# Kernel tuning notes

Hardware: AMD Instinct MI355X
Metric: run time of the kernel (lower is better)

The kernel has to match this reference:

```python
import jax, jax.numpy as jnp
import numpy as np
from string import ascii_letters as ABC

N = 12
DIM = 2 ** N
_s = 1.0 / np.sqrt(2.0)
# measurement-basis rotations for X, Y, Z
U_BASIS = jnp.asarray(np.stack([
    np.array([[1, 1], [1, -1]]) * _s,
    np.array([[1, -1j], [1, 1j]]) * _s,
    np.eye(2),
]), dtype=jnp.complex64)


def build_H(params_x, params_zz):
    """Dense transverse-field Ising Hamiltonian: sum_i x_i X_i + sum_i zz_i Z_i Z_{i+1}."""
    basis = jnp.arange(DIM)
    bits = (basis[:, None] >> jnp.arange(N)[None, :]) & 1          # (DIM, N)
    signs = (1 - 2 * bits).astype(jnp.float32)                      # Z eigenvalues
    zz_diag = (signs[:, :-1] * signs[:, 1:]) @ params_zz            # (DIM,)
    flips = basis[:, None] ^ (1 << jnp.arange(N))[None, :]          # (DIM, N)
    rows = jnp.repeat(basis, N)
    cols = flips.reshape(-1)
    vals = jnp.tile(params_x, DIM).astype(jnp.complex64)
    H = jnp.zeros((DIM, DIM), jnp.complex64).at[rows, cols].add(vals)
    return H + jnp.diag(zz_diag.astype(jnp.complex64))


def setup_inputs() -> dict:
    key = jax.random.key(0)
    k1, k2, k3, k4, k5 = jax.random.split(key, 5)
    return {
        "initial_state": 0,
        "ts": jax.random.uniform(k1, (8,), dtype=jnp.float32),
        "pauli_obs": jax.random.randint(k2, (32, N), 0, 3),
        "indices": jax.random.randint(k3, (8, 32, 256), 0, DIM),
        "params_x": jax.random.normal(k4, (N,), dtype=jnp.float32),
        "params_zz": jax.random.normal(k5, (N - 1,), dtype=jnp.float32),
    }


def reference(initial_state, ts, pauli_obs, indices, params_x, params_zz):
    H = build_H(params_x, params_zz)
    rots = U_BASIS[pauli_obs]                    # (B, N, 2, 2)
    ops = [rots[:, i] for i in range(N)]
    subs = ','.join([ABC[1:1 + N]] + [f'a{ABC[1 + N + i]}{ABC[1 + i]}' for i in range(N)]) \
        + '->a' + ABC[1 + N:1 + 2 * N]
    B = pauli_obs.shape[0]

    def one_t(args):
        t, idx = args
        U = jax.scipy.linalg.expm((-1j) * t.astype(jnp.complex64) * H)
        fs = U[:, initial_state].reshape([2] * N)          # state tensor
        rot_state = jnp.einsum(subs, fs, *ops)             # (B, 2, ..., 2)
        probs = jnp.abs(rot_state.reshape(B, DIM)) ** 2    # (B, DIM)
        return jnp.take_along_axis(probs, idx, axis=1)     # (B, shots)

    return jax.lax.map(one_t, (ts, indices))               # (T, B, shots)
```

## Files before the change

### kernel.cpp

```cpp
#include <hip/hip_runtime.h>
#include <math.h>

#define QN 12
#define QDIM 4096
#define CHEB_TOL 2e-3f
#define LSZ (QDIM + 2 * (QDIM / 16))

template <int CTRL>
__device__ __forceinline__ float dppf(float x) {
    int v = __builtin_amdgcn_update_dpp(0, __float_as_int(x), CTRL, 0xF, 0xF, false);
    return __int_as_float(v);
}
#define DPP_QX1 0xB1
#define DPP_QX2 0x4E
#define DPP_QX3 0x1B
#define DPP_HM  0x141
#define DPP_R8  0x128
__device__ __forceinline__ float dpp_x1(float x) { return dppf<DPP_QX1>(x); }
__device__ __forceinline__ float dpp_x2(float x) { return dppf<DPP_QX2>(x); }
__device__ __forceinline__ float dpp_x4(float x) { return dppf<DPP_HM>(dppf<DPP_QX3>(x)); }
__device__ __forceinline__ float dpp_x8(float x) { return dppf<DPP_R8>(x); }

#define CHEB_STEP(T1, T2, CURB, NXTB, KVAL, FVAL, ODD, WRITEB)                \
    {                                                                          \
        const int   k_ = (KVAL);                                               \
        const float f_ = (FVAL);                                               \
        float4 nbv[6][2];                                                      \
        _Pragma("unroll")                                                      \
        for (int j = 6; j < QN; ++j) {                                         \
            const int gx = g0 ^ (1 << j);                                      \
            const int hx = h0 ^ (1 << (j - 4));                                \
            const float4* q4 = (const float4*)((CURB) + gx + 2 * hx);          \
            nbv[j - 6][0] = q4[0];                                             \
            nbv[j - 6][1] = q4[1];                                             \
        }                                                                      \
        float hr[4], hi[4];                                                    \
        _Pragma("unroll")                                                      \
        for (int e = 0; e < 4; ++e) {                                          \
            hr[e] = dg[e] * T1[e].x + xj[0] * T1[e ^ 1].x                      \
                  + xj[1] * T1[e ^ 2].x;                                       \
            hi[e] = dg[e] * T1[e].y + xj[0] * T1[e ^ 1].y                      \
                  + xj[1] * T1[e ^ 2].y;                                       \
            hr[e] += xj[2] * dpp_x1(T1[e].x);  hi[e] += xj[2] * dpp_x1(T1[e].y); \
            hr[e] += xj[3] * dpp_x2(T1[e].x);  hi[e] += xj[3] * dpp_x2(T1[e].y); \
            hr[e] += xj[4] * dpp_x4(T1[e].x);  hi[e] += xj[4] * dpp_x4(T1[e].y); \
            hr[e] += xj[5] * dpp_x8(T1[e].x);  hi[e] += xj[5] * dpp_x8(T1[e].y); \
        }                                                                      \
        _Pragma("unroll")                                                      \
        for (int j = 6; j < QN; ++j) {                                         \
            _Pragma("unroll")                                                  \
            for (int m = 0; m < 2; ++m) {                                      \
                hr[2 * m]     += xj[j] * nbv[j - 6][m].x;                      \
                hi[2 * m]     += xj[j] * nbv[j - 6][m].y;                      \
                hr[2 * m + 1] += xj[j] * nbv[j - 6][m].z;                      \
                hi[2 * m + 1] += xj[j] * nbv[j - 6][m].w;                      \
            }                                                                  \
        }                                                                      \
        const float Jk2 = 2.0f * Jc[k_];                                       \
        const float c_  = (k_ & 2) ? Jk2 : -Jk2;                               \
        _Pragma("unroll")                                                      \
        for (int e = 0; e < 4; ++e) {                                          \
            const float tnx = f_ * hr[e] - T2[e].x;                            \
            const float tny = f_ * hi[e] - T2[e].y;                            \
            T2[e].x = tnx; T2[e].y = tny;                                      \
            if (ODD) {                                                         \
                acc[e].x = fmaf(-c_, tny, acc[e].x);                           \
                acc[e].y = fmaf( c_, tnx, acc[e].y);                           \
            } else {                                                           \
                acc[e].x = fmaf(-c_, tnx, acc[e].x);                           \
                acc[e].y = fmaf(-c_, tny, acc[e].y);                           \
            }                                                                  \
        }                                                                      \
        if (WRITEB) {                                                          \
            float4* w_ = (float4*)((NXTB) + l0);                               \
            w_[0] = make_float4(T2[0].x, T2[0].y, T2[1].x, T2[1].y);           \
            w_[1] = make_float4(T2[2].x, T2[2].y, T2[3].x, T2[3].y);           \
            __syncthreads();                                                   \
        }                                                                      \
    }

__global__ __launch_bounds__(1024) void evolve_kernel(
    const int* __restrict__ init_state,
    const float* __restrict__ ts,
    const float* __restrict__ params_x,
    const float* __restrict__ params_zz,
    float2* __restrict__ psi_out)
{
    __shared__ __align__(16) float2 bufA[LSZ];
    __shared__ __align__(16) float2 bufB[LSZ];
    __shared__ float  Jc[128];
    __shared__ float  suLDS[160];
    __shared__ int    dsh;

    const int tid = threadIdx.x;
    const int tI  = blockIdx.x;
    const float t = ts[tI];
    const int g0 = tid * 4;
    const int h0 = g0 >> 4;
    const int l0 = g0 + 2 * h0;

    if (tid < 160) suLDS[tid] = 0.f;

    float xj[QN];
    float bound = 0.f;
#pragma unroll
    for (int j = 0; j < QN; ++j) { xj[j] = params_x[j]; bound += fabsf(xj[j]); }
    float zz[QN - 1];
#pragma unroll
    for (int i = 0; i < QN - 1; ++i) { zz[i] = params_zz[i]; bound += fabsf(zz[i]); }

    float dg[4];
#pragma unroll
    for (int e = 0; e < 4; ++e) {
        const int g = g0 + e;
        float dv = 0.f;
#pragma unroll
        for (int i = 0; i < QN - 1; ++i) {
            const int flip = ((g >> i) ^ (g >> (i + 1))) & 1;
            dv += zz[i] * (1.0f - 2.0f * (float)flip);
        }
        dg[e] = dv;
    }

    const float theta = t * bound;
    int dmax = (int)ceilf(theta + 5.0f * cbrtf(theta)) + 6;
    if (dmax < 8) dmax = 8;
    if (dmax > 126) dmax = 126;

    {
        const int M = dmax + 24;
        const double th = (double)fmaxf(theta, 1e-6f);
        const double invth = 1.0 / th;
        double jkp1 = 0.0, jk = 1e-30, mine = 0.0, nrm = 0.0, suf = 0.0, su_own = 0.0;
        for (int k = M; k >= 0; --k) {
            suf += fabs(jk);
            if (k == tid) { mine = jk; su_own = suf; }
            if (k == 0) nrm += jk;
            else if ((k & 1) == 0) nrm += 2.0 * jk;
            const double jkm1 = (2.0 * (double)k * invth) * jk - jkp1;
            jkp1 = jk; jk = jkm1;
            if (fabs(jk) > 1e250) {
                jk *= 1e-250; jkp1 *= 1e-250; mine *= 1e-250;
                nrm *= 1e-250; suf *= 1e-250; su_own *= 1e-250;
            }
        }
        const double anrm = fabs(nrm);
        if (tid <= dmax) Jc[tid] = (float)(mine / nrm);
        if (tid < 160) suLDS[tid] = (float)(su_own / anrm);
    }

    const int is = init_state[0];
    const float inv_s = 1.0f / bound;

    float2 ta[4];
    float2 tb[4];
    float2 acc[4];
#pragma unroll
    for (int e = 0; e < 4; ++e) {
        const float v = (g0 + e == is) ? 1.0f : 0.0f;
        ta[e] = make_float2(v, 0.f);
        tb[e] = make_float2(0.f, 0.f);
    }
    {
        float4* w0 = (float4*)(bufA + l0);
        w0[0] = make_float4(ta[0].x, ta[0].y, ta[1].x, ta[1].y);
        w0[1] = make_float4(ta[2].x, ta[2].y, ta[3].x, ta[3].y);
    }
    __syncthreads();

    if (tid < 64) {
        const bool p0 = suLDS[tid + 1] < CHEB_TOL;
        const bool p1 = suLDS[tid + 65] < CHEB_TOL;
        const unsigned long long b0 = __ballot(p0);
        const unsigned long long b1 = __ballot(p1);
        if (tid == 0) {
            int dd;
            if (b0) dd = __ffsll(b0) - 1;
            else if (b1) dd = 64 + __ffsll(b1) - 1;
            else dd = dmax;
            if (dd < 2) dd = 2;
            if (dd > dmax) dd = dmax;
            dsh = dd;
        }
    }
    __syncthreads();
    const int d = dsh;

#pragma unroll
    for (int e = 0; e < 4; ++e) acc[e] = make_float2(Jc[0] * ta[e].x, 0.f);

    CHEB_STEP(ta, tb, bufA, bufB, 1, inv_s, true, (1 < d));
    const float f2 = 2.0f * inv_s;
    int k = 2;
    for (; k + 1 <= d; k += 2) {
        CHEB_STEP(tb, ta, bufB, bufA, k,     f2, false, true);
        CHEB_STEP(ta, tb, bufA, bufB, k + 1, f2, true,  (k + 1 < d));
    }
    if (k <= d) {
        CHEB_STEP(tb, ta, bufB, bufA, k, f2, false, false);
    }

    float4* o = (float4*)(psi_out + tI * QDIM + g0);
    o[0] = make_float4(acc[0].x, acc[0].y, acc[1].x, acc[1].y);
    o[1] = make_float4(acc[2].x, acc[2].y, acc[3].x, acc[3].y);
}

__global__ __launch_bounds__(512) void measure_kernel(
    const float2* __restrict__ psi,
    const int* __restrict__ pauli_obs,
    const int* __restrict__ indices,
    float* __restrict__ out)
{
    __shared__ float2 st[QDIM];
    const int blk = blockIdx.x;
    const int tI = blk >> 5;
    const int b  = blk & 31;

    const float4* src = (const float4*)(psi + tI * QDIM);
    float4* dst = (float4*)st;
    for (int i = threadIdx.x; i < QDIM / 2; i += 512) dst[i] = src[i];
    __syncthreads();

    const float s = 0.70710678118654752440f;
    for (int q = 0; q < QN; ++q) {
        const int p = pauli_obs[b * QN + (QN - 1 - q)];
        if (p == 2) continue;
        const int mask = 1 << q;
        for (int it = threadIdx.x; it < QDIM / 2; it += 512) {
            const int gl = ((it & ~(mask - 1)) << 1) | (it & (mask - 1));
            const int gh = gl | mask;
            const float2 a  = st[gl];
            const float2 c2 = st[gh];
            float2 r0, r1;
            if (p == 0) {
                r0 = make_float2(s * (a.x + c2.x), s * (a.y + c2.y));
                r1 = make_float2(s * (a.x - c2.x), s * (a.y - c2.y));
            } else {
                r0 = make_float2(s * (a.x + c2.y), s * (a.y - c2.x));
                r1 = make_float2(s * (a.x - c2.y), s * (a.y + c2.x));
            }
            st[gl] = r0;
            st[gh] = r1;
        }
        __syncthreads();
    }

    if (threadIdx.x < 256) {
        const int oi = (tI * 32 + b) * 256 + threadIdx.x;
        const int idx = indices[oi];
        const float2 v = st[idx];
        out[oi] = v.x * v.x + v.y * v.y;
    }
}

extern "C" void kernel_launch(void* const* d_in, const int* in_sizes, int n_in,
                              void* d_out, int out_size, void* d_ws, size_t ws_size,
                              hipStream_t stream) {
    const int*   init_state = (const int*)d_in[0];
    const float* ts         = (const float*)d_in[1];
    const int*   pauli_obs  = (const int*)d_in[2];
    const int*   indices    = (const int*)d_in[3];
    const float* params_x   = (const float*)d_in[4];
    const float* params_zz  = (const float*)d_in[5];
    float*  out = (float*)d_out;
    float2* psi = (float2*)d_ws;

    hipLaunchKernelGGL(evolve_kernel, dim3(8), dim3(1024), 0, stream,
                       init_state, ts, params_x, params_zz, psi);
    hipLaunchKernelGGL(measure_kernel, dim3(8 * 32), dim3(512), 0, stream,
                       psi, pauli_obs, indices, out);
}
```

Baseline: 116.3 us.

## Use permlane swaps for qubits 6-7 and fuse qubit pairs in measurement

In the Chebyshev evolve step, the neighbours for qubits 6 and 7 are now fetched with the permlane16/permlane32 swap cross-lane instructions instead of LDS reads. This drops two of the six LDS neighbour reads per step. The measurement kernel now applies basis rotations two qubits at a time, using a padded LDS layout and 1024 threads with four amplitudes per thread. That halves the number of barrier-separated passes and cuts bank conflicts. The costs are reliance on gfx950-specific permlane builtins and more complex index math.

```diff
diff --git a/kernel.cpp b/kernel.cpp
--- a/kernel.cpp
+++ b/kernel.cpp
@@ -5,6 +5,8 @@
 #define QDIM 4096
 #define CHEB_TOL 2e-3f
 #define LSZ (QDIM + 2 * (QDIM / 16))
+
+typedef unsigned int uint2_v __attribute__((ext_vector_type(2)));
 
 template <int CTRL>
 __device__ __forceinline__ float dppf(float x) {
@@ -21,18 +23,29 @@
 __device__ __forceinline__ float dpp_x4(float x) { return dppf<DPP_HM>(dppf<DPP_QX3>(x)); }
 __device__ __forceinline__ float dpp_x8(float x) { return dppf<DPP_R8>(x); }
 
+__device__ __forceinline__ float pl16(float x, bool rowodd) {
+    uint2_v r = __builtin_amdgcn_permlane16_swap(
+        __float_as_uint(x), __float_as_uint(x), false, false);
+    return __uint_as_float(rowodd ? r[0] : r[1]);
+}
+__device__ __forceinline__ float pl32(float x, bool hihalf) {
+    uint2_v r = __builtin_amdgcn_permlane32_swap(
+        __float_as_uint(x), __float_as_uint(x), false, false);
+    return __uint_as_float(hihalf ? r[0] : r[1]);
+}
+
 #define CHEB_STEP(T1, T2, CURB, NXTB, KVAL, FVAL, ODD, WRITEB)                \
     {                                                                          \
         const int   k_ = (KVAL);                                               \
         const float f_ = (FVAL);                                               \
-        float4 nbv[6][2];                                                      \
+        float4 nbv[4][2];                                                      \
         _Pragma("unroll")                                                      \
-        for (int j = 6; j < QN; ++j) {                                         \
+        for (int j = 8; j < QN; ++j) {                                         \
             const int gx = g0 ^ (1 << j);                                      \
             const int hx = h0 ^ (1 << (j - 4));                                \
             const float4* q4 = (const float4*)((CURB) + gx + 2 * hx);          \
-            nbv[j - 6][0] = q4[0];                                             \
-            nbv[j - 6][1] = q4[1];                                             \
+            nbv[j - 8][0] = q4[0];                                             \
+            nbv[j - 8][1] = q4[1];                                             \
         }                                                                      \
         float hr[4], hi[4];                                                    \
         _Pragma("unroll")                                                      \
@@ -45,15 +58,17 @@
             hr[e] += xj[3] * dpp_x2(T1[e].x);  hi[e] += xj[3] * dpp_x2(T1[e].y); \
             hr[e] += xj[4] * dpp_x4(T1[e].x);  hi[e] += xj[4] * dpp_x4(T1[e].y); \
             hr[e] += xj[5] * dpp_x8(T1[e].x);  hi[e] += xj[5] * dpp_x8(T1[e].y); \
+            hr[e] += xj[6] * pl16(T1[e].x, sel16); hi[e] += xj[6] * pl16(T1[e].y, sel16); \
+            hr[e] += xj[7] * pl32(T1[e].x, sel32); hi[e] += xj[7] * pl32(T1[e].y, sel32); \
         }                                                                      \
         _Pragma("unroll")                                                      \
-        for (int j = 6; j < QN; ++j) {                                         \
+        for (int j = 8; j < QN; ++j) {                                         \
             _Pragma("unroll")                                                  \
             for (int m = 0; m < 2; ++m) {                                      \
-                hr[2 * m]     += xj[j] * nbv[j - 6][m].x;                      \
-                hi[2 * m]     += xj[j] * nbv[j - 6][m].y;                      \
-                hr[2 * m + 1] += xj[j] * nbv[j - 6][m].z;                      \
-                hi[2 * m + 1] += xj[j] * nbv[j - 6][m].w;                      \
+                hr[2 * m]     += xj[j] * nbv[j - 8][m].x;                      \
+                hi[2 * m]     += xj[j] * nbv[j - 8][m].y;                      \
+                hr[2 * m + 1] += xj[j] * nbv[j - 8][m].z;                      \
+                hi[2 * m + 1] += xj[j] * nbv[j - 8][m].w;                      \
             }                                                                  \
         }                                                                      \
         const float Jk2 = 2.0f * Jc[k_];                                       \
@@ -98,6 +113,8 @@
     const int g0 = tid * 4;
     const int h0 = g0 >> 4;
     const int l0 = g0 + 2 * h0;
+    const bool sel16 = (tid >> 4) & 1;
+    const bool sel32 = (tid >> 5) & 1;
 
     if (tid < 160) suLDS[tid] = 0.f;
 
@@ -205,51 +222,79 @@
     o[1] = make_float4(acc[2].x, acc[2].y, acc[3].x, acc[3].y);
 }
 
-__global__ __launch_bounds__(512) void measure_kernel(
+__device__ __forceinline__ void apply_g(int p, float2& lo, float2& hi) {
+    const float s = 0.70710678118654752440f;
+    const float2 a = lo, c = hi;
+    if (p == 0) {
+        lo = make_float2(s * (a.x + c.x), s * (a.y + c.y));
+        hi = make_float2(s * (a.x - c.x), s * (a.y - c.y));
+    } else if (p == 1) {
+        lo = make_float2(s * (a.x + c.y), s * (a.y - c.x));
+        hi = make_float2(s * (a.x - c.y), s * (a.y + c.x));
+    }
+}
+
+__global__ __launch_bounds__(1024) void measure_kernel(
     const float2* __restrict__ psi,
     const int* __restrict__ pauli_obs,
     const int* __restrict__ indices,
     float* __restrict__ out)
 {
-    __shared__ float2 st[QDIM];
+    __shared__ __align__(16) float2 st[LSZ];
+    const int tid = threadIdx.x;
     const int blk = blockIdx.x;
     const int tI = blk >> 5;
     const int b  = blk & 31;
 
-    const float4* src = (const float4*)(psi + tI * QDIM);
-    float4* dst = (float4*)st;
-    for (int i = threadIdx.x; i < QDIM / 2; i += 512) dst[i] = src[i];
+    const int g0 = tid * 4;
+    const int l0 = g0 + 2 * (g0 >> 4);
+    {
+        const float4* src = (const float4*)(psi + tI * QDIM + g0);
+        float4* w = (float4*)(st + l0);
+        w[0] = src[0];
+        w[1] = src[1];
+    }
     __syncthreads();
 
-    const float s = 0.70710678118654752440f;
-    for (int q = 0; q < QN; ++q) {
-        const int p = pauli_obs[b * QN + (QN - 1 - q)];
-        if (p == 2) continue;
-        const int mask = 1 << q;
-        for (int it = threadIdx.x; it < QDIM / 2; it += 512) {
-            const int gl = ((it & ~(mask - 1)) << 1) | (it & (mask - 1));
-            const int gh = gl | mask;
-            const float2 a  = st[gl];
-            const float2 c2 = st[gh];
-            float2 r0, r1;
-            if (p == 0) {
-                r0 = make_float2(s * (a.x + c2.x), s * (a.y + c2.y));
-                r1 = make_float2(s * (a.x - c2.x), s * (a.y - c2.y));
-            } else {
-                r0 = make_float2(s * (a.x + c2.y), s * (a.y - c2.x));
-                r1 = make_float2(s * (a.x - c2.y), s * (a.y + c2.x));
+#pragma unroll
+    for (int qp = 0; qp < QN / 2; ++qp) {
+        const int qa = 2 * qp;
+        const int pa = pauli_obs[b * QN + (QN - 1 - qa)];
+        const int pb = pauli_obs[b * QN + (QN - 2 - qa)];
+        if (pa == 2 && pb == 2) continue;
+        float2 v[4];
+        if (qa == 0) {
+            float4* r = (float4*)(st + l0);
+            const float4 r0 = r[0], r1 = r[1];
+            v[0] = make_float2(r0.x, r0.y); v[1] = make_float2(r0.z, r0.w);
+            v[2] = make_float2(r1.x, r1.y); v[3] = make_float2(r1.z, r1.w);
+            apply_g(pa, v[0], v[1]); apply_g(pa, v[2], v[3]);
+            apply_g(pb, v[0], v[2]); apply_g(pb, v[1], v[3]);
+            r[0] = make_float4(v[0].x, v[0].y, v[1].x, v[1].y);
+            r[1] = make_float4(v[2].x, v[2].y, v[3].x, v[3].y);
+        } else {
+            const int m = (1 << qa) - 1;
+            const int base = ((tid & ~m) << 2) | (tid & m);
+            int li[4];
+#pragma unroll
+            for (int kk = 0; kk < 4; ++kk) {
+                const int g = base + (kk << qa);
+                li[kk] = g + 2 * (g >> 4);
+                v[kk] = st[li[kk]];
             }
-            st[gl] = r0;
-            st[gh] = r1;
+            apply_g(pa, v[0], v[1]); apply_g(pa, v[2], v[3]);
+            apply_g(pb, v[0], v[2]); apply_g(pb, v[1], v[3]);
+#pragma unroll
+            for (int kk = 0; kk < 4; ++kk) st[li[kk]] = v[kk];
         }
         __syncthreads();
     }
 
-    if (threadIdx.x < 256) {
-        const int oi = (tI * 32 + b) * 256 + threadIdx.x;
+    if (tid < 256) {
+        const int oi = (tI * 32 + b) * 256 + tid;
         const int idx = indices[oi];
-        const float2 v = st[idx];
-        out[oi] = v.x * v.x + v.y * v.y;
+        const float2 vv = st[idx + 2 * (idx >> 4)];
+        out[oi] = vv.x * vv.x + vv.y * vv.y;
     }
 }
 
@@ -267,6 +312,6 @@
 
     hipLaunchKernelGGL(evolve_kernel, dim3(8), dim3(1024), 0, stream,
                        init_state, ts, params_x, params_zz, psi);
-    hipLaunchKernelGGL(measure_kernel, dim3(8 * 32), dim3(512), 0, stream,
+    hipLaunchKernelGGL(measure_kernel, dim3(8 * 32), dim3(1024), 0, stream,
                        psi, pauli_obs, indices, out);
 }
```

Result: slower. 128.8 us (+10.7%).
